# Optimization experiments

Hardware: AMD Instinct MI355X
Metric: run time of the kernel (lower is better)

The kernel has to match this reference:

```python
import jax, jax.numpy as jnp
import numpy as np

N_NODES = 100000
N_EDGES = 3200000
K = 10
ALPHA = 0.1


def setup_inputs() -> dict:
    key = jax.random.key(0)
    k1, k2, k3, k4 = jax.random.split(key, 4)
    x = jax.random.normal(k1, (N_NODES, 512), dtype=jnp.float32)
    edge_index = jax.random.randint(k2, (2, N_EDGES), 0, N_NODES, dtype=jnp.int64)
    W1 = jax.random.normal(k3, (512, 16), dtype=jnp.float32) * 0.05
    b1 = jnp.zeros((16,), dtype=jnp.float32)
    W2 = jax.random.normal(k4, (16, 64), dtype=jnp.float32) * 0.05
    b2 = jnp.zeros((64,), dtype=jnp.float32)
    return {"x": x, "W1": W1, "b1": b1, "W2": W2, "b2": b2,
            "edge_index": edge_index}


def reference(x, W1, b1, W2, b2, edge_index):
    n = x.shape[0]
    # MLP encoder
    h = jax.nn.relu(x @ W1 + b1)          # [N, 16]
    h = h @ W2 + b2                       # [N, C]
    # gcn_norm with self-loops (PyG default for APPNP)
    self_idx = jnp.arange(n, dtype=edge_index.dtype)
    row = jnp.concatenate([edge_index[0], self_idx])   # source nodes
    col = jnp.concatenate([edge_index[1], self_idx])   # target nodes
    deg = jax.ops.segment_sum(jnp.ones_like(col, dtype=h.dtype), col, num_segments=n)
    dinv = jnp.where(deg > 0, jax.lax.rsqrt(deg), 0.0)
    norm = dinv[row] * dinv[col]          # [E+N]
    # APPNP: K steps of x <- (1-a) * A_hat x + a * x0
    h0 = h
    def step(h, _):
        agg = jax.ops.segment_sum(norm[:, None] * h[row], col, num_segments=n)
        return (1.0 - ALPHA) * agg + ALPHA * h0, None
    h, _ = jax.lax.scan(step, h, None, length=K)
    return jax.nn.log_softmax(h, axis=1)
```

## Files before the change

### kernel.cpp

```cpp
#include <hip/hip_runtime.h>
#include <hip/hip_bf16.h>
#include <hip/hip_fp16.h>


typedef unsigned short u16;
typedef __attribute__((ext_vector_type(8))) short short8;
typedef __attribute__((ext_vector_type(4))) float f32x4;
typedef __attribute__((ext_vector_type(4))) unsigned u32x4;

#define WPB 4
#define BSH2 9
#define BN2 512
#define NBMAX 200
#define CAP 20480
#define SCWG 392

__device__ __forceinline__ float loadF(const void* p, size_t i, int bf) {
  if (bf) return __bfloat162float(((const __hip_bfloat16*)p)[i]);
  return ((const float*)p)[i];
}
__device__ __forceinline__ float blo(unsigned u) {
  return __uint_as_float(u << 16);
}
__device__ __forceinline__ float bhi(unsigned u) {
  return __uint_as_float(u & 0xffff0000u);
}
__device__ __forceinline__ u16 f2b(float v) {
  __hip_bfloat16 b = __float2bfloat16(v);
  return *reinterpret_cast<u16*>(&b);
}
__device__ __forceinline__ unsigned pk2(float lo, float hi) {
  return (unsigned)f2b(lo) | ((unsigned)f2b(hi) << 16);
}
__device__ __forceinline__ int clampN(int v, int N) {
  v = v < 0 ? 0 : v;
  return v >= N ? N - 1 : v;
}
__device__ __forceinline__ float nrm_of(unsigned e) {
  return __half2float(__ushort_as_half((unsigned short)(e & 0x7fffu)));
}

__global__ void detect_k(const void* x, const int* ei, int* flags) {
  __shared__ int red[2];
  const int tid = threadIdx.x;
  if (tid < 2) red[tid] = 0;
  __syncthreads();
  const __hip_bfloat16* xb = (const __hip_bfloat16*)x;
  float v = __bfloat162float(xb[tid]);
  int sane = (v == v && fabsf(v) < 64.f) ? 1 : 0;
  int zer = (ei[2 * tid + 1] == 0) ? 1 : 0;
  atomicAdd(&red[0], sane);
  atomicAdd(&red[1], zer);
  __syncthreads();
  if (tid == 0) {
    flags[0] = (red[0] >= 1024 - 32) ? 1 : 0;
    flags[1] = (red[1] >= 1024 - 128) ? 1 : 0;
  }
}

__global__ __launch_bounds__(256) void scat_k(
    const int* __restrict__ ei, int E, int N, int NB,
    int* __restrict__ gcur, uint2* __restrict__ bpair,
    const int* __restrict__ flags) {
  __shared__ int hist[NBMAX];
  __shared__ int resv[NBMAX];
  const int tid = threadIdx.x;
  const int chunk = (E + SCWG - 1) / SCWG;
  const int e0 = blockIdx.x * chunk;
  const int e1 = min(e0 + chunk, E);
  if (e0 >= E) return;
  const int wide = flags[1];
  for (int i = tid; i < NB; i += 256) hist[i] = 0;
  __syncthreads();
  for (int e = e0 + tid; e < e1; e += 256) {
    int c = wide ? ei[2 * ((long)E + e)] : ei[(long)E + e];
    atomicAdd(&hist[clampN(c, N) >> BSH2], 1);
  }
  __syncthreads();
  for (int b = tid; b < NB; b += 256) {
    int cnt = hist[b];
    resv[b] = cnt ? atomicAdd(&gcur[b], cnt) : 0;
  }
  __syncthreads();
  for (int i = tid; i < NB; i += 256) hist[i] = 0;
  __syncthreads();
  for (int e = e0 + tid; e < e1; e += 256) {
    int r = wide ? ei[2 * (long)e] : ei[e];
    int c = wide ? ei[2 * ((long)E + e)] : ei[(long)E + e];
    r = clampN(r, N); c = clampN(c, N);
    const int b = c >> BSH2;
    const int pos = resv[b] + atomicAdd(&hist[b], 1);
    if (pos < CAP)
      bpair[(size_t)b * CAP + pos] = make_uint2((unsigned)r, (unsigned)c);
  }
}

__global__ void bscan_k(const int* __restrict__ gcur, int NB,
                        int* __restrict__ cbase) {
  if (threadIdx.x == 0) {
    int s = 0;
    for (int b = 0; b < NB; b++) {
      cbase[b] = s;
      s += min(gcur[b], CAP);
    }
    cbase[NB] = s;
  }
}

__global__ __launch_bounds__(1024) void fill2a_k(
    const uint2* __restrict__ bpair, const int* __restrict__ gcur,
    const int* __restrict__ cbase, int* __restrict__ colptr,
    float* __restrict__ dinv, int N, int NB) {
  __shared__ int lhist[BN2];
  __shared__ int pref[BN2];
  const int b = blockIdx.x;
  const int tid = threadIdx.x;
  const int nb0 = b << BSH2;
  const int nn = min(BN2, N - nb0);
  if (tid < BN2) lhist[tid] = 0;
  __syncthreads();
  const size_t wbeg = (size_t)b * CAP;
  const int cnt = min(gcur[b], CAP);
  for (int i = tid; i < cnt; i += 1024) {
    int dl = (int)bpair[wbeg + i].y - nb0;
    atomicAdd(&lhist[dl], 1);
  }
  __syncthreads();
  if (tid < BN2) pref[tid] = lhist[tid];
  __syncthreads();
  for (int off = 1; off < BN2; off <<= 1) {
    int v = 0;
    if (tid < BN2 && tid >= off) v = pref[tid - off];
    __syncthreads();
    if (tid < BN2) pref[tid] += v;
    __syncthreads();
  }
  if (tid < nn) {
    const int excl = pref[tid] - lhist[tid];
    colptr[nb0 + tid] = cbase[b] + excl;
    dinv[nb0 + tid] = rsqrtf(1.0f + (float)lhist[tid]);
  }
  if (b == NB - 1 && tid == 0) colptr[N] = cbase[NB];
}

__global__ __launch_bounds__(1024) void fill2b_k(
    const uint2* __restrict__ bpair, const int* __restrict__ gcur,
    const int* __restrict__ colptr, const float* __restrict__ dinv,
    unsigned* __restrict__ epk, int N, int NB) {
  __shared__ int lcur[BN2];
  __shared__ float ldv[BN2];
  const int b = blockIdx.x;
  const int tid = threadIdx.x;
  const int nb0 = b << BSH2;
  const int nn = min(BN2, N - nb0);
  if (tid < nn) {
    lcur[tid] = colptr[nb0 + tid];
    ldv[tid] = dinv[nb0 + tid];
  }
  __syncthreads();
  const size_t wbeg = (size_t)b * CAP;
  const int cnt = min(gcur[b], CAP);
  for (int i = tid; i < cnt; i += 1024) {
    const uint2 p = bpair[wbeg + i];
    const int dl = (int)p.y - nb0;
    const int slot = atomicAdd(&lcur[dl], 1);
    const float nrm = dinv[p.x] * ldv[dl];
    epk[slot] = (p.x << 15) | (unsigned)__half_as_ushort(__float2half(nrm));
  }
}

__global__ __launch_bounds__(256) void mlp_k(
    const void* __restrict__ x, const void* __restrict__ W1,
    const void* __restrict__ b1, const int* __restrict__ flags,
    u16* __restrict__ h10, u16* __restrict__ pha, float* __restrict__ sa,
    int N) {
  __shared__ __align__(16) short Blds[8192];
  __shared__ float b1s[16];
  __shared__ float h1s[WPB][16][17];

  const int tid = threadIdx.x;
  const int f0 = flags[0];

  for (int idx = tid; idx < 8192; idx += 256) {
    int ks = idx >> 9, ln = (idx >> 3) & 63, j = idx & 7;
    int k = ks * 32 + ((ln >> 4) << 3) + j;
    int n = ln & 15;
    float w = loadF(W1, (size_t)k * 16 + n, f0);
    Blds[idx] = (short)f2b(w);
  }
  if (tid < 16) b1s[tid] = loadF(b1, tid, f0);
  __syncthreads();

  const int lane = tid & 63;
  const int wv = tid >> 6;
  const int tile = (blockIdx.x * WPB + wv) * 16;
  if (tile >= N) return;

  const int m = lane & 15;
  const int quad = lane >> 4;
  const int row = min(tile + m, N - 1);
  const size_t rowbase = (size_t)row * 512 + (quad << 3);

  f32x4 acc = {0.f, 0.f, 0.f, 0.f};
  if (f0) {
    short8 af[16];
#pragma unroll
    for (int ks = 0; ks < 16; ks++)
      af[ks] = *reinterpret_cast<const short8*>((const u16*)x + rowbase + ks * 32);
#pragma unroll
    for (int ks = 0; ks < 16; ks++) {
      const short8 bf = *reinterpret_cast<const short8*>(&Blds[(ks * 64 + lane) * 8]);
      acc = __builtin_amdgcn_mfma_f32_16x16x32_bf16(af[ks], bf, acc, 0, 0, 0);
    }
  } else {
#pragma unroll
    for (int ks = 0; ks < 16; ks++) {
      short8 a;
      const float* xf = (const float*)x + rowbase + ks * 32;
      const float4 lo = *reinterpret_cast<const float4*>(xf);
      const float4 hi = *reinterpret_cast<const float4*>(xf + 4);
      a[0] = (short)f2b(lo.x); a[1] = (short)f2b(lo.y);
      a[2] = (short)f2b(lo.z); a[3] = (short)f2b(lo.w);
      a[4] = (short)f2b(hi.x); a[5] = (short)f2b(hi.y);
      a[6] = (short)f2b(hi.z); a[7] = (short)f2b(hi.w);
      const short8 bf = *reinterpret_cast<const short8*>(&Blds[(ks * 64 + lane) * 8]);
      acc = __builtin_amdgcn_mfma_f32_16x16x32_bf16(a, bf, acc, 0, 0, 0);
    }
  }

#pragma unroll
  for (int r = 0; r < 4; r++)
    h1s[wv][quad * 4 + r][m] = fmaxf(acc[r] + b1s[m], 0.f);

  const int node = lane >> 2;
  const int gnode = tile + node;
  if (gnode < N) {
    const int cp = (lane & 3) << 2;
    uint2 pv;
    pv.x = pk2(h1s[wv][node][cp + 0], h1s[wv][node][cp + 1]);
    pv.y = pk2(h1s[wv][node][cp + 2], h1s[wv][node][cp + 3]);
    *reinterpret_cast<uint2*>(h10 + (((size_t)gnode) << 4) + cp) = pv;
    *reinterpret_cast<uint2*>(pha + (((size_t)gnode) << 4) + cp) = pv;
    if ((lane & 3) == 0) sa[gnode] = 1.0f;
  }
}

__global__ __launch_bounds__(256) void gather_k(
    const u16* __restrict__ hcur, const float* __restrict__ scur,
    const u16* __restrict__ h10, const int* __restrict__ colptr,
    const unsigned* __restrict__ epk, const float* __restrict__ dinv,
    u16* __restrict__ hnext, float* __restrict__ snext, int N) {
  const int gw = (int)((blockIdx.x * 256u + threadIdx.x) >> 6);
  if (gw >= N) return;
  const int lane = threadIdx.x & 63;
  const int es = lane >> 2;
  const int q = lane & 3;
  const int co = q << 2;
  const int beg = __builtin_amdgcn_readfirstlane(colptr[gw]);
  const int end = __builtin_amdgcn_readfirstlane(colptr[gw + 1]);

  float a0 = 0.f, a1 = 0.f, a2 = 0.f, a3 = 0.f, as = 0.f;
  float c0 = 0.f, c1 = 0.f, c2 = 0.f, c3 = 0.f, cs = 0.f;
  int t = beg + es;
  for (; t + 16 < end; t += 32) {
    const unsigned e0 = __builtin_nontemporal_load(epk + t);
    const unsigned e1 = __builtin_nontemporal_load(epk + t + 16);
    const unsigned i0 = e0 >> 15, i1 = e1 >> 15;
    const uint2 u0 = *reinterpret_cast<const uint2*>(hcur + (((size_t)i0) << 4) + co);
    const uint2 u1 = *reinterpret_cast<const uint2*>(hcur + (((size_t)i1) << 4) + co);
    const float sv0 = scur[i0], sv1 = scur[i1];
    const float n0 = nrm_of(e0), n1 = nrm_of(e1);
    a0 = fmaf(n0, blo(u0.x), a0); a1 = fmaf(n0, bhi(u0.x), a1);
    a2 = fmaf(n0, blo(u0.y), a2); a3 = fmaf(n0, bhi(u0.y), a3);
    as = fmaf(n0, sv0, as);
    c0 = fmaf(n1, blo(u1.x), c0); c1 = fmaf(n1, bhi(u1.x), c1);
    c2 = fmaf(n1, blo(u1.y), c2); c3 = fmaf(n1, bhi(u1.y), c3);
    cs = fmaf(n1, sv1, cs);
  }
  if (t < end) {
    const unsigned e0 = __builtin_nontemporal_load(epk + t);
    const unsigned i0 = e0 >> 15;
    const uint2 u0 = *reinterpret_cast<const uint2*>(hcur + (((size_t)i0) << 4) + co);
    const float sv0 = scur[i0];
    const float n0 = nrm_of(e0);
    a0 = fmaf(n0, blo(u0.x), a0); a1 = fmaf(n0, bhi(u0.x), a1);
    a2 = fmaf(n0, blo(u0.y), a2); a3 = fmaf(n0, bhi(u0.y), a3);
    as = fmaf(n0, sv0, as);
  }
  a0 += c0; a1 += c1; a2 += c2; a3 += c3; as += cs;
#pragma unroll
  for (int d = 4; d <= 32; d <<= 1) {
    a0 += __shfl_xor(a0, d, 64); a1 += __shfl_xor(a1, d, 64);
    a2 += __shfl_xor(a2, d, 64); a3 += __shfl_xor(a3, d, 64);
    as += __shfl_xor(as, d, 64);
  }
  if (es == 0) {
    const size_t base = (((size_t)gw) << 4) + co;
    const uint2 hs = *reinterpret_cast<const uint2*>(hcur + base);
    const uint2 hz = *reinterpret_cast<const uint2*>(h10 + base);
    const float di = dinv[gw];
    const float dd = di * di;
    const float r0 = 0.9f * (a0 + dd * blo(hs.x)) + 0.1f * blo(hz.x);
    const float r1 = 0.9f * (a1 + dd * bhi(hs.x)) + 0.1f * bhi(hz.x);
    const float r2 = 0.9f * (a2 + dd * blo(hs.y)) + 0.1f * blo(hz.y);
    const float r3 = 0.9f * (a3 + dd * bhi(hs.y)) + 0.1f * bhi(hz.y);
    uint2 pv;
    pv.x = pk2(r0, r1); pv.y = pk2(r2, r3);
    *reinterpret_cast<uint2*>(hnext + base) = pv;
    if (q == 0) snext[gw] = 0.9f * (as + dd * scur[gw]) + 0.1f;
  }
}

__global__ __launch_bounds__(256) void out_k(
    const u16* __restrict__ ph1, const float* __restrict__ s,
    const void* __restrict__ W2, const void* __restrict__ b2,
    void* __restrict__ out, const int* __restrict__ flags, int N) {
  __shared__ float W2s[16 * 64];
  __shared__ float b2s[64];
  const int tid = threadIdx.x;
  const int f0 = flags[0];
  for (int i = tid; i < 1024; i += 256) W2s[i] = loadF(W2, i, f0);
  if (tid < 64) b2s[tid] = loadF(b2, tid, f0);
  __syncthreads();
  const int gw = (int)((blockIdx.x * 256u + tid) >> 6);
  if (gw >= N) return;
  const int lane = tid & 63;
  const u16* row = ph1 + (((size_t)gw) << 4);
  const u32x4 ua = *reinterpret_cast<const u32x4*>(row);
  const u32x4 ub = *reinterpret_cast<const u32x4*>(row + 8);
  float h[16];
  h[0] = blo(ua[0]);  h[1] = bhi(ua[0]);  h[2] = blo(ua[1]);  h[3] = bhi(ua[1]);
  h[4] = blo(ua[2]);  h[5] = bhi(ua[2]);  h[6] = blo(ua[3]);  h[7] = bhi(ua[3]);
  h[8] = blo(ub[0]);  h[9] = bhi(ub[0]);  h[10] = blo(ub[1]); h[11] = bhi(ub[1]);
  h[12] = blo(ub[2]); h[13] = bhi(ub[2]); h[14] = blo(ub[3]); h[15] = bhi(ub[3]);
  float v = s[gw] * b2s[lane];
#pragma unroll
  for (int j = 0; j < 16; j++) v = fmaf(h[j], W2s[(j << 6) + lane], v);
  float m = v;
#pragma unroll
  for (int off = 32; off; off >>= 1) m = fmaxf(m, __shfl_xor(m, off, 64));
  float e = __expf(v - m);
  float ssum = e;
#pragma unroll
  for (int off = 32; off; off >>= 1) ssum += __shfl_xor(ssum, off, 64);
  const float r = v - m - __logf(ssum);
  const size_t o = (((size_t)gw) << 6) + lane;
  if (f0) ((__hip_bfloat16*)out)[o] = __float2bfloat16(r);
  else ((float*)out)[o] = r;
}

extern "C" void kernel_launch(void* const* d_in, const int* in_sizes, int n_in,
                              void* d_out, int out_size, void* d_ws, size_t ws_size,
                              hipStream_t stream) {
  (void)n_in; (void)out_size; (void)ws_size;
  const void* x  = d_in[0];
  const void* W1 = d_in[1];
  const void* b1 = d_in[2];
  const void* W2 = d_in[3];
  const void* b2 = d_in[4];
  const int* ei  = (const int*)d_in[5];

  const int N = in_sizes[0] / 512;
  const int E = in_sizes[5] / 2;
  const int NB = (N + BN2 - 1) >> BSH2;

  char* w = (char*)d_ws;
  size_t off = 0;
  auto alloc = [&](size_t bytes) -> void* {
    void* p = w + off;
    off += (bytes + 255) & ~(size_t)255;
    return p;
  };
  const size_t h16b = (size_t)N * 16 * 2;
  const size_t sb_  = ((size_t)N * 4 + 255) & ~(size_t)255;
  const size_t propb = 3 * ((h16b + 255) & ~(size_t)255) + 2 * sb_;
  const size_t bpb = (size_t)NB * CAP * 8;
  char*  regionA = (char*)alloc(propb > bpb ? propb : bpb);
  const size_t h16a = (h16b + 255) & ~(size_t)255;
  u16*   h10 = (u16*)regionA;
  u16*   pha = (u16*)(regionA + h16a);
  u16*   phb = (u16*)(regionA + 2 * h16a);
  float* sa  = (float*)(regionA + 3 * h16a);
  float* sb  = (float*)(regionA + 3 * h16a + sb_);
  uint2* bpair  = (uint2*)regionA;
  unsigned* epk = (unsigned*)alloc((size_t)E * 4);
  int*   colptr = (int*)alloc(((size_t)N + 1) * 4);
  float* dinv   = (float*)alloc((size_t)N * 4);
  int*   gcur   = (int*)alloc((size_t)NB * 4);
  int*   cbase  = (int*)alloc(((size_t)NB + 1) * 4);
  int*   flags  = (int*)alloc(256);

  hipMemsetAsync(gcur, 0, (size_t)NB * 4, stream);
  detect_k<<<1, 1024, 0, stream>>>(x, ei, flags);
  scat_k<<<SCWG, 256, 0, stream>>>(ei, E, N, NB, gcur, bpair, flags);
  bscan_k<<<1, 64, 0, stream>>>(gcur, NB, cbase);
  fill2a_k<<<NB, 1024, 0, stream>>>(bpair, gcur, cbase, colptr, dinv, N, NB);
  fill2b_k<<<NB, 1024, 0, stream>>>(bpair, gcur, colptr, dinv, epk, N, NB);
  mlp_k<<<(N + 63) / 64, 256, 0, stream>>>(x, W1, b1, flags, h10, pha, sa, N);

  const int gblocks = (N + WPB - 1) / WPB;
  for (int it = 0; it < 10; ++it) {
    if ((it & 1) == 0)
      gather_k<<<gblocks, 256, 0, stream>>>(pha, sa, h10, colptr, epk, dinv,
                                            phb, sb, N);
    else
      gather_k<<<gblocks, 256, 0, stream>>>(phb, sb, h10, colptr, epk, dinv,
                                            pha, sa, N);
  }
  out_k<<<gblocks, 256, 0, stream>>>(pha, sa, W2, b2, d_out, flags, N);
}
```

Measured before the change: 1.045 ms.

## Replace CSR per-node gather with per-bucket LDS atomic accumulation

Drops the CSR build (colptr prefix scan and slot scatter) and stores edges unsorted within each 512-node destination bucket as (src, local dst | fp16 norm) pairs. Propagation now runs one 1024-thread block per bucket that gathers each source row and accumulates into shared-memory float arrays with LDS atomics, then applies the APPNP update. The goal is to cut preprocessing work and use full-row vector loads. In exchange, edge storage doubles to 8 bytes and each iteration pays 17 LDS atomics per edge, with possible contention. Launching only about 196 blocks may also leave the GPU underused.

```diff
diff --git a/kernel.cpp b/kernel.cpp
--- a/kernel.cpp
+++ b/kernel.cpp
@@ -35,9 +35,6 @@
 __device__ __forceinline__ int clampN(int v, int N) {
   v = v < 0 ? 0 : v;
   return v >= N ? N - 1 : v;
-}
-__device__ __forceinline__ float nrm_of(unsigned e) {
-  return __half2float(__ushort_as_half((unsigned short)(e & 0x7fffu)));
 }
 
 __global__ void detect_k(const void* x, const int* ei, int* flags) {
@@ -107,12 +104,10 @@
   }
 }
 
-__global__ __launch_bounds__(1024) void fill2a_k(
+__global__ __launch_bounds__(1024) void deg_k(
     const uint2* __restrict__ bpair, const int* __restrict__ gcur,
-    const int* __restrict__ cbase, int* __restrict__ colptr,
     float* __restrict__ dinv, int N, int NB) {
   __shared__ int lhist[BN2];
-  __shared__ int pref[BN2];
   const int b = blockIdx.x;
   const int tid = threadIdx.x;
   const int nb0 = b << BSH2;
@@ -121,51 +116,33 @@
   __syncthreads();
   const size_t wbeg = (size_t)b * CAP;
   const int cnt = min(gcur[b], CAP);
-  for (int i = tid; i < cnt; i += 1024) {
-    int dl = (int)bpair[wbeg + i].y - nb0;
-    atomicAdd(&lhist[dl], 1);
-  }
-  __syncthreads();
-  if (tid < BN2) pref[tid] = lhist[tid];
-  __syncthreads();
-  for (int off = 1; off < BN2; off <<= 1) {
-    int v = 0;
-    if (tid < BN2 && tid >= off) v = pref[tid - off];
-    __syncthreads();
-    if (tid < BN2) pref[tid] += v;
-    __syncthreads();
-  }
-  if (tid < nn) {
-    const int excl = pref[tid] - lhist[tid];
-    colptr[nb0 + tid] = cbase[b] + excl;
-    dinv[nb0 + tid] = rsqrtf(1.0f + (float)lhist[tid]);
-  }
-  if (b == NB - 1 && tid == 0) colptr[N] = cbase[NB];
-}
-
-__global__ __launch_bounds__(1024) void fill2b_k(
+  for (int i = tid; i < cnt; i += 1024)
+    atomicAdd(&lhist[clampN((int)bpair[wbeg + i].y - nb0, BN2)], 1);
+  __syncthreads();
+  if (tid < nn) dinv[nb0 + tid] = rsqrtf(1.0f + (float)lhist[tid]);
+}
+
+__global__ __launch_bounds__(1024) void pack_k(
     const uint2* __restrict__ bpair, const int* __restrict__ gcur,
-    const int* __restrict__ colptr, const float* __restrict__ dinv,
-    unsigned* __restrict__ epk, int N, int NB) {
-  __shared__ int lcur[BN2];
+    const int* __restrict__ cbase, const float* __restrict__ dinv,
+    uint2* __restrict__ epk2, int N, int NB) {
   __shared__ float ldv[BN2];
   const int b = blockIdx.x;
   const int tid = threadIdx.x;
   const int nb0 = b << BSH2;
   const int nn = min(BN2, N - nb0);
-  if (tid < nn) {
-    lcur[tid] = colptr[nb0 + tid];
-    ldv[tid] = dinv[nb0 + tid];
-  }
+  if (tid < nn) ldv[tid] = dinv[nb0 + tid];
   __syncthreads();
   const size_t wbeg = (size_t)b * CAP;
   const int cnt = min(gcur[b], CAP);
+  const int obase = cbase[b];
   for (int i = tid; i < cnt; i += 1024) {
     const uint2 p = bpair[wbeg + i];
-    const int dl = (int)p.y - nb0;
-    const int slot = atomicAdd(&lcur[dl], 1);
+    const int dl = clampN((int)p.y - nb0, BN2);
     const float nrm = dinv[p.x] * ldv[dl];
-    epk[slot] = (p.x << 15) | (unsigned)__half_as_ushort(__float2half(nrm));
+    const unsigned h16 =
+        (unsigned)__half_as_ushort(__float2half(nrm));
+    epk2[obase + i] = make_uint2(p.x, ((unsigned)dl << 16) | h16);
   }
 }
 
@@ -245,69 +222,69 @@
   }
 }
 
-__global__ __launch_bounds__(256) void gather_k(
+__global__ __launch_bounds__(1024) void gatherB_k(
     const u16* __restrict__ hcur, const float* __restrict__ scur,
-    const u16* __restrict__ h10, const int* __restrict__ colptr,
-    const unsigned* __restrict__ epk, const float* __restrict__ dinv,
-    u16* __restrict__ hnext, float* __restrict__ snext, int N) {
-  const int gw = (int)((blockIdx.x * 256u + threadIdx.x) >> 6);
-  if (gw >= N) return;
-  const int lane = threadIdx.x & 63;
-  const int es = lane >> 2;
-  const int q = lane & 3;
-  const int co = q << 2;
-  const int beg = __builtin_amdgcn_readfirstlane(colptr[gw]);
-  const int end = __builtin_amdgcn_readfirstlane(colptr[gw + 1]);
-
-  float a0 = 0.f, a1 = 0.f, a2 = 0.f, a3 = 0.f, as = 0.f;
-  float c0 = 0.f, c1 = 0.f, c2 = 0.f, c3 = 0.f, cs = 0.f;
-  int t = beg + es;
-  for (; t + 16 < end; t += 32) {
-    const unsigned e0 = __builtin_nontemporal_load(epk + t);
-    const unsigned e1 = __builtin_nontemporal_load(epk + t + 16);
-    const unsigned i0 = e0 >> 15, i1 = e1 >> 15;
-    const uint2 u0 = *reinterpret_cast<const uint2*>(hcur + (((size_t)i0) << 4) + co);
-    const uint2 u1 = *reinterpret_cast<const uint2*>(hcur + (((size_t)i1) << 4) + co);
-    const float sv0 = scur[i0], sv1 = scur[i1];
-    const float n0 = nrm_of(e0), n1 = nrm_of(e1);
-    a0 = fmaf(n0, blo(u0.x), a0); a1 = fmaf(n0, bhi(u0.x), a1);
-    a2 = fmaf(n0, blo(u0.y), a2); a3 = fmaf(n0, bhi(u0.y), a3);
-    as = fmaf(n0, sv0, as);
-    c0 = fmaf(n1, blo(u1.x), c0); c1 = fmaf(n1, bhi(u1.x), c1);
-    c2 = fmaf(n1, blo(u1.y), c2); c3 = fmaf(n1, bhi(u1.y), c3);
-    cs = fmaf(n1, sv1, cs);
-  }
-  if (t < end) {
-    const unsigned e0 = __builtin_nontemporal_load(epk + t);
-    const unsigned i0 = e0 >> 15;
-    const uint2 u0 = *reinterpret_cast<const uint2*>(hcur + (((size_t)i0) << 4) + co);
-    const float sv0 = scur[i0];
-    const float n0 = nrm_of(e0);
-    a0 = fmaf(n0, blo(u0.x), a0); a1 = fmaf(n0, bhi(u0.x), a1);
-    a2 = fmaf(n0, blo(u0.y), a2); a3 = fmaf(n0, bhi(u0.y), a3);
-    as = fmaf(n0, sv0, as);
-  }
-  a0 += c0; a1 += c1; a2 += c2; a3 += c3; as += cs;
-#pragma unroll
-  for (int d = 4; d <= 32; d <<= 1) {
-    a0 += __shfl_xor(a0, d, 64); a1 += __shfl_xor(a1, d, 64);
-    a2 += __shfl_xor(a2, d, 64); a3 += __shfl_xor(a3, d, 64);
-    as += __shfl_xor(as, d, 64);
-  }
-  if (es == 0) {
-    const size_t base = (((size_t)gw) << 4) + co;
-    const uint2 hs = *reinterpret_cast<const uint2*>(hcur + base);
-    const uint2 hz = *reinterpret_cast<const uint2*>(h10 + base);
-    const float di = dinv[gw];
+    const u16* __restrict__ h10, const uint2* __restrict__ epk2,
+    const int* __restrict__ cbase, const int* __restrict__ gcur,
+    const float* __restrict__ dinv, u16* __restrict__ hnext,
+    float* __restrict__ snext, int N, int NB) {
+  __shared__ float acc[BN2][17];
+  __shared__ float sacc[BN2];
+  const int b = blockIdx.x;
+  const int tid = threadIdx.x;
+  const int nb0 = b << BSH2;
+  for (int i = tid; i < BN2 * 17; i += 1024)
+    (&acc[0][0])[i] = 0.f;
+  for (int i = tid; i < BN2; i += 1024) sacc[i] = 0.f;
+  __syncthreads();
+
+  const int cnt = min(gcur[b], CAP);
+  const int e0 = cbase[b];
+  for (int i = tid; i < cnt; i += 1024) {
+    const uint2 p = epk2[e0 + i];
+    const unsigned src = p.x;
+    const int dl = (int)(p.y >> 16);
+    const float nrm =
+        __half2float(__ushort_as_half((unsigned short)(p.y & 0xffffu)));
+    const u16* row = hcur + ((size_t)src << 4);
+    const u32x4 ua = *reinterpret_cast<const u32x4*>(row);
+    const u32x4 ub = *reinterpret_cast<const u32x4*>(row + 8);
+    float* ap = acc[dl];
+    atomicAdd(&ap[0],  nrm * blo(ua[0])); atomicAdd(&ap[1],  nrm * bhi(ua[0]));
+    atomicAdd(&ap[2],  nrm * blo(ua[1])); atomicAdd(&ap[3],  nrm * bhi(ua[1]));
+    atomicAdd(&ap[4],  nrm * blo(ua[2])); atomicAdd(&ap[5],  nrm * bhi(ua[2]));
+    atomicAdd(&ap[6],  nrm * blo(ua[3])); atomicAdd(&ap[7],  nrm * bhi(ua[3]));
+    atomicAdd(&ap[8],  nrm * blo(ub[0])); atomicAdd(&ap[9],  nrm * bhi(ub[0]));
+    atomicAdd(&ap[10], nrm * blo(ub[1])); atomicAdd(&ap[11], nrm * bhi(ub[1]));
+    atomicAdd(&ap[12], nrm * blo(ub[2])); atomicAdd(&ap[13], nrm * bhi(ub[2]));
+    atomicAdd(&ap[14], nrm * blo(ub[3])); atomicAdd(&ap[15], nrm * bhi(ub[3]));
+    atomicAdd(&sacc[dl], nrm * scur[src]);
+  }
+  __syncthreads();
+
+  const int tgt = tid >> 1;
+  const int ho = (tid & 1) << 3;
+  const int node = nb0 + tgt;
+  if (node < N) {
+    const float di = dinv[node];
     const float dd = di * di;
-    const float r0 = 0.9f * (a0 + dd * blo(hs.x)) + 0.1f * blo(hz.x);
-    const float r1 = 0.9f * (a1 + dd * bhi(hs.x)) + 0.1f * bhi(hz.x);
-    const float r2 = 0.9f * (a2 + dd * blo(hs.y)) + 0.1f * blo(hz.y);
-    const float r3 = 0.9f * (a3 + dd * bhi(hs.y)) + 0.1f * bhi(hz.y);
-    uint2 pv;
-    pv.x = pk2(r0, r1); pv.y = pk2(r2, r3);
-    *reinterpret_cast<uint2*>(hnext + base) = pv;
-    if (q == 0) snext[gw] = 0.9f * (as + dd * scur[gw]) + 0.1f;
+    const size_t base = (((size_t)node) << 4) + ho;
+    const u32x4 hs = *reinterpret_cast<const u32x4*>(hcur + base);
+    const u32x4 hz = *reinterpret_cast<const u32x4*>(h10 + base);
+    const float* ap = acc[tgt] + ho;
+    const float r0 = 0.9f * (ap[0] + dd * blo(hs[0])) + 0.1f * blo(hz[0]);
+    const float r1 = 0.9f * (ap[1] + dd * bhi(hs[0])) + 0.1f * bhi(hz[0]);
+    const float r2 = 0.9f * (ap[2] + dd * blo(hs[1])) + 0.1f * blo(hz[1]);
+    const float r3 = 0.9f * (ap[3] + dd * bhi(hs[1])) + 0.1f * bhi(hz[1]);
+    const float r4 = 0.9f * (ap[4] + dd * blo(hs[2])) + 0.1f * blo(hz[2]);
+    const float r5 = 0.9f * (ap[5] + dd * bhi(hs[2])) + 0.1f * bhi(hz[2]);
+    const float r6 = 0.9f * (ap[6] + dd * blo(hs[3])) + 0.1f * blo(hz[3]);
+    const float r7 = 0.9f * (ap[7] + dd * bhi(hs[3])) + 0.1f * bhi(hz[3]);
+    u32x4 pv;
+    pv[0] = pk2(r0, r1); pv[1] = pk2(r2, r3);
+    pv[2] = pk2(r4, r5); pv[3] = pk2(r6, r7);
+    *reinterpret_cast<u32x4*>(hnext + base) = pv;
+    if (ho == 0) snext[node] = 0.9f * (sacc[tgt] + dd * scur[node]) + 0.1f;
   }
 }
 
@@ -383,8 +360,7 @@
   float* sa  = (float*)(regionA + 3 * h16a);
   float* sb  = (float*)(regionA + 3 * h16a + sb_);
   uint2* bpair  = (uint2*)regionA;
-  unsigned* epk = (unsigned*)alloc((size_t)E * 4);
-  int*   colptr = (int*)alloc(((size_t)N + 1) * 4);
+  uint2* epk2   = (uint2*)alloc((size_t)E * 8);
   float* dinv   = (float*)alloc((size_t)N * 4);
   int*   gcur   = (int*)alloc((size_t)NB * 4);
   int*   cbase  = (int*)alloc(((size_t)NB + 1) * 4);
@@ -394,18 +370,18 @@
   detect_k<<<1, 1024, 0, stream>>>(x, ei, flags);
   scat_k<<<SCWG, 256, 0, stream>>>(ei, E, N, NB, gcur, bpair, flags);
   bscan_k<<<1, 64, 0, stream>>>(gcur, NB, cbase);
-  fill2a_k<<<NB, 1024, 0, stream>>>(bpair, gcur, cbase, colptr, dinv, N, NB);
-  fill2b_k<<<NB, 1024, 0, stream>>>(bpair, gcur, colptr, dinv, epk, N, NB);
+  deg_k<<<NB, 1024, 0, stream>>>(bpair, gcur, dinv, N, NB);
+  pack_k<<<NB, 1024, 0, stream>>>(bpair, gcur, cbase, dinv, epk2, N, NB);
   mlp_k<<<(N + 63) / 64, 256, 0, stream>>>(x, W1, b1, flags, h10, pha, sa, N);
 
-  const int gblocks = (N + WPB - 1) / WPB;
   for (int it = 0; it < 10; ++it) {
     if ((it & 1) == 0)
-      gather_k<<<gblocks, 256, 0, stream>>>(pha, sa, h10, colptr, epk, dinv,
-                                            phb, sb, N);
+      gatherB_k<<<NB, 1024, 0, stream>>>(pha, sa, h10, epk2, cbase, gcur,
+                                         dinv, phb, sb, N, NB);
     else
-      gather_k<<<gblocks, 256, 0, stream>>>(phb, sb, h10, colptr, epk, dinv,
-                                            pha, sa, N);
-  }
+      gatherB_k<<<NB, 1024, 0, stream>>>(phb, sb, h10, epk2, cbase, gcur,
+                                         dinv, pha, sa, N, NB);
+  }
+  const int gblocks = (N + WPB - 1) / WPB;
   out_k<<<gblocks, 256, 0, stream>>>(pha, sa, W2, b2, d_out, flags, N);
 }
```

After: 4.090 ms. 291% more time.

## Interleave bias-scale scalar into padded 64-byte node rows and parallelize bucket scan

Applied to the files above, without the earlier changes.

Each node's 16 bf16 features and its propagated bias-scale scalar now share one 64-byte padded row, so the gather fetches the scalar from the same cache line as the features instead of from a separate array. This removes a second random memory access per edge in every propagation step, at the cost of doubling the footprint of the feature buffers. The single-thread serial bucket prefix scan is also replaced by a 256-thread shared-memory Hillis-Steele scan, which assumes at most 256 buckets.

```diff
diff --git a/kernel.cpp b/kernel.cpp
--- a/kernel.cpp
+++ b/kernel.cpp
@@ -95,16 +95,21 @@
   }
 }
 
-__global__ void bscan_k(const int* __restrict__ gcur, int NB,
-                        int* __restrict__ cbase) {
-  if (threadIdx.x == 0) {
-    int s = 0;
-    for (int b = 0; b < NB; b++) {
-      cbase[b] = s;
-      s += min(gcur[b], CAP);
-    }
-    cbase[NB] = s;
-  }
+__global__ __launch_bounds__(256) void bscan_k(const int* __restrict__ gcur,
+                                               int NB, int* __restrict__ cbase) {
+  __shared__ int v[256];
+  const int tid = threadIdx.x;
+  const int x = (tid < NB) ? min(gcur[tid], CAP) : 0;
+  v[tid] = x;
+  __syncthreads();
+  for (int off = 1; off < 256; off <<= 1) {
+    int t = (tid >= off) ? v[tid - off] : 0;
+    __syncthreads();
+    v[tid] += t;
+    __syncthreads();
+  }
+  if (tid < NB) cbase[tid] = v[tid] - x;
+  if (tid == NB - 1) cbase[NB] = v[tid];
 }
 
 __global__ __launch_bounds__(1024) void fill2a_k(
@@ -172,8 +177,7 @@
 __global__ __launch_bounds__(256) void mlp_k(
     const void* __restrict__ x, const void* __restrict__ W1,
     const void* __restrict__ b1, const int* __restrict__ flags,
-    u16* __restrict__ h10, u16* __restrict__ pha, float* __restrict__ sa,
-    int N) {
+    u16* __restrict__ h10, u16* __restrict__ pha, int N) {
   __shared__ __align__(16) short Blds[8192];
   __shared__ float b1s[16];
   __shared__ float h1s[WPB][16][17];
@@ -239,17 +243,20 @@
     uint2 pv;
     pv.x = pk2(h1s[wv][node][cp + 0], h1s[wv][node][cp + 1]);
     pv.y = pk2(h1s[wv][node][cp + 2], h1s[wv][node][cp + 3]);
-    *reinterpret_cast<uint2*>(h10 + (((size_t)gnode) << 4) + cp) = pv;
-    *reinterpret_cast<uint2*>(pha + (((size_t)gnode) << 4) + cp) = pv;
-    if ((lane & 3) == 0) sa[gnode] = 1.0f;
+    const size_t rb = ((size_t)gnode) << 5;
+    *reinterpret_cast<uint2*>(h10 + rb + cp) = pv;
+    *reinterpret_cast<uint2*>(pha + rb + cp) = pv;
+    if ((lane & 3) == 0) {
+      *reinterpret_cast<float*>(h10 + rb + 16) = 1.0f;
+      *reinterpret_cast<float*>(pha + rb + 16) = 1.0f;
+    }
   }
 }
 
 __global__ __launch_bounds__(256) void gather_k(
-    const u16* __restrict__ hcur, const float* __restrict__ scur,
-    const u16* __restrict__ h10, const int* __restrict__ colptr,
-    const unsigned* __restrict__ epk, const float* __restrict__ dinv,
-    u16* __restrict__ hnext, float* __restrict__ snext, int N) {
+    const u16* __restrict__ hcur, const u16* __restrict__ h10,
+    const int* __restrict__ colptr, const unsigned* __restrict__ epk,
+    const float* __restrict__ dinv, u16* __restrict__ hnext, int N) {
   const int gw = (int)((blockIdx.x * 256u + threadIdx.x) >> 6);
   if (gw >= N) return;
   const int lane = threadIdx.x & 63;
@@ -265,10 +272,12 @@
   for (; t + 16 < end; t += 32) {
     const unsigned e0 = __builtin_nontemporal_load(epk + t);
     const unsigned e1 = __builtin_nontemporal_load(epk + t + 16);
-    const unsigned i0 = e0 >> 15, i1 = e1 >> 15;
-    const uint2 u0 = *reinterpret_cast<const uint2*>(hcur + (((size_t)i0) << 4) + co);
-    const uint2 u1 = *reinterpret_cast<const uint2*>(hcur + (((size_t)i1) << 4) + co);
-    const float sv0 = scur[i0], sv1 = scur[i1];
+    const u16* r0 = hcur + (((size_t)(e0 >> 15)) << 5);
+    const u16* r1 = hcur + (((size_t)(e1 >> 15)) << 5);
+    const uint2 u0 = *reinterpret_cast<const uint2*>(r0 + co);
+    const uint2 u1 = *reinterpret_cast<const uint2*>(r1 + co);
+    const float sv0 = *reinterpret_cast<const float*>(r0 + 16);
+    const float sv1 = *reinterpret_cast<const float*>(r1 + 16);
     const float n0 = nrm_of(e0), n1 = nrm_of(e1);
     a0 = fmaf(n0, blo(u0.x), a0); a1 = fmaf(n0, bhi(u0.x), a1);
     a2 = fmaf(n0, blo(u0.y), a2); a3 = fmaf(n0, bhi(u0.y), a3);
@@ -279,9 +288,9 @@
   }
   if (t < end) {
     const unsigned e0 = __builtin_nontemporal_load(epk + t);
-    const unsigned i0 = e0 >> 15;
-    const uint2 u0 = *reinterpret_cast<const uint2*>(hcur + (((size_t)i0) << 4) + co);
-    const float sv0 = scur[i0];
+    const u16* r0 = hcur + (((size_t)(e0 >> 15)) << 5);
+    const uint2 u0 = *reinterpret_cast<const uint2*>(r0 + co);
+    const float sv0 = *reinterpret_cast<const float*>(r0 + 16);
     const float n0 = nrm_of(e0);
     a0 = fmaf(n0, blo(u0.x), a0); a1 = fmaf(n0, bhi(u0.x), a1);
     a2 = fmaf(n0, blo(u0.y), a2); a3 = fmaf(n0, bhi(u0.y), a3);
@@ -295,9 +304,11 @@
     as += __shfl_xor(as, d, 64);
   }
   if (es == 0) {
-    const size_t base = (((size_t)gw) << 4) + co;
-    const uint2 hs = *reinterpret_cast<const uint2*>(hcur + base);
-    const uint2 hz = *reinterpret_cast<const uint2*>(h10 + base);
+    const size_t rb = ((size_t)gw) << 5;
+    const uint2 hs = *reinterpret_cast<const uint2*>(hcur + rb + co);
+    const uint2 hz = *reinterpret_cast<const uint2*>(h10 + rb + co);
+    const float ss = *reinterpret_cast<const float*>(hcur + rb + 16);
+    const float sz = *reinterpret_cast<const float*>(h10 + rb + 16);
     const float di = dinv[gw];
     const float dd = di * di;
     const float r0 = 0.9f * (a0 + dd * blo(hs.x)) + 0.1f * blo(hz.x);
@@ -306,15 +317,17 @@
     const float r3 = 0.9f * (a3 + dd * bhi(hs.y)) + 0.1f * bhi(hz.y);
     uint2 pv;
     pv.x = pk2(r0, r1); pv.y = pk2(r2, r3);
-    *reinterpret_cast<uint2*>(hnext + base) = pv;
-    if (q == 0) snext[gw] = 0.9f * (as + dd * scur[gw]) + 0.1f;
+    *reinterpret_cast<uint2*>(hnext + rb + co) = pv;
+    if (q == 0)
+      *reinterpret_cast<float*>(hnext + rb + 16) =
+          0.9f * (as + dd * ss) + 0.1f * sz;
   }
 }
 
 __global__ __launch_bounds__(256) void out_k(
-    const u16* __restrict__ ph1, const float* __restrict__ s,
-    const void* __restrict__ W2, const void* __restrict__ b2,
-    void* __restrict__ out, const int* __restrict__ flags, int N) {
+    const u16* __restrict__ ph1, const void* __restrict__ W2,
+    const void* __restrict__ b2, void* __restrict__ out,
+    const int* __restrict__ flags, int N) {
   __shared__ float W2s[16 * 64];
   __shared__ float b2s[64];
   const int tid = threadIdx.x;
@@ -325,15 +338,16 @@
   const int gw = (int)((blockIdx.x * 256u + tid) >> 6);
   if (gw >= N) return;
   const int lane = tid & 63;
-  const u16* row = ph1 + (((size_t)gw) << 4);
+  const u16* row = ph1 + (((size_t)gw) << 5);
   const u32x4 ua = *reinterpret_cast<const u32x4*>(row);
   const u32x4 ub = *reinterpret_cast<const u32x4*>(row + 8);
+  const float s = *reinterpret_cast<const float*>(row + 16);
   float h[16];
   h[0] = blo(ua[0]);  h[1] = bhi(ua[0]);  h[2] = blo(ua[1]);  h[3] = bhi(ua[1]);
   h[4] = blo(ua[2]);  h[5] = bhi(ua[2]);  h[6] = blo(ua[3]);  h[7] = bhi(ua[3]);
   h[8] = blo(ub[0]);  h[9] = bhi(ub[0]);  h[10] = blo(ub[1]); h[11] = bhi(ub[1]);
   h[12] = blo(ub[2]); h[13] = bhi(ub[2]); h[14] = blo(ub[3]); h[15] = bhi(ub[3]);
-  float v = s[gw] * b2s[lane];
+  float v = s * b2s[lane];
 #pragma unroll
   for (int j = 0; j < 16; j++) v = fmaf(h[j], W2s[(j << 6) + lane], v);
   float m = v;
@@ -371,17 +385,13 @@
     off += (bytes + 255) & ~(size_t)255;
     return p;
   };
-  const size_t h16b = (size_t)N * 16 * 2;
-  const size_t sb_  = ((size_t)N * 4 + 255) & ~(size_t)255;
-  const size_t propb = 3 * ((h16b + 255) & ~(size_t)255) + 2 * sb_;
+  const size_t hrow = ((size_t)N * 64 + 255) & ~(size_t)255;
+  const size_t propb = 3 * hrow;
   const size_t bpb = (size_t)NB * CAP * 8;
   char*  regionA = (char*)alloc(propb > bpb ? propb : bpb);
-  const size_t h16a = (h16b + 255) & ~(size_t)255;
   u16*   h10 = (u16*)regionA;
-  u16*   pha = (u16*)(regionA + h16a);
-  u16*   phb = (u16*)(regionA + 2 * h16a);
-  float* sa  = (float*)(regionA + 3 * h16a);
-  float* sb  = (float*)(regionA + 3 * h16a + sb_);
+  u16*   pha = (u16*)(regionA + hrow);
+  u16*   phb = (u16*)(regionA + 2 * hrow);
   uint2* bpair  = (uint2*)regionA;
   unsigned* epk = (unsigned*)alloc((size_t)E * 4);
   int*   colptr = (int*)alloc(((size_t)N + 1) * 4);
@@ -393,19 +403,17 @@
   hipMemsetAsync(gcur, 0, (size_t)NB * 4, stream);
   detect_k<<<1, 1024, 0, stream>>>(x, ei, flags);
   scat_k<<<SCWG, 256, 0, stream>>>(ei, E, N, NB, gcur, bpair, flags);
-  bscan_k<<<1, 64, 0, stream>>>(gcur, NB, cbase);
+  bscan_k<<<1, 256, 0, stream>>>(gcur, NB, cbase);
   fill2a_k<<<NB, 1024, 0, stream>>>(bpair, gcur, cbase, colptr, dinv, N, NB);
   fill2b_k<<<NB, 1024, 0, stream>>>(bpair, gcur, colptr, dinv, epk, N, NB);
-  mlp_k<<<(N + 63) / 64, 256, 0, stream>>>(x, W1, b1, flags, h10, pha, sa, N);
+  mlp_k<<<(N + 63) / 64, 256, 0, stream>>>(x, W1, b1, flags, h10, pha, N);
 
   const int gblocks = (N + WPB - 1) / WPB;
   for (int it = 0; it < 10; ++it) {
     if ((it & 1) == 0)
-      gather_k<<<gblocks, 256, 0, stream>>>(pha, sa, h10, colptr, epk, dinv,
-                                            phb, sb, N);
+      gather_k<<<gblocks, 256, 0, stream>>>(pha, h10, colptr, epk, dinv, phb, N);
     else
-      gather_k<<<gblocks, 256, 0, stream>>>(phb, sb, h10, colptr, epk, dinv,
-                                            pha, sa, N);
-  }
-  out_k<<<gblocks, 256, 0, stream>>>(pha, sa, W2, b2, d_out, flags, N);
-}
+      gather_k<<<gblocks, 256, 0, stream>>>(phb, h10, colptr, epk, dinv, pha, N);
+  }
+  out_k<<<gblocks, 256, 0, stream>>>(pha, W2, b2, d_out, flags, N);
+}
```

New measurement: 1.030 ms. No clear change (-1.4%).
